# Optimization experiments

Measured on AMD Instinct MI355X. Metric: run time of the kernel, lower is better.

## Reference

```python
import jax, jax.numpy as jnp
import numpy as np

N_NODES = 100000
N_EDGES = 1600000
IN_DIM = 128
OUT_DIM = 64


def setup_inputs() -> dict:
    key = jax.random.key(0)
    k1, k2, k3, k4, k5 = jax.random.split(key, 5)
    return {
        "h_init": jax.random.normal(k1, (N_NODES, IN_DIM), dtype=jnp.float32),
        "W1": jax.random.normal(k2, (OUT_DIM, IN_DIM), dtype=jnp.float32),
        "a": jax.random.normal(k3, (1, OUT_DIM), dtype=jnp.float32),
        "src": jax.random.randint(k4, (N_EDGES,), 0, N_NODES, dtype=jnp.int64)
        if jax.config.jax_enable_x64 else jax.random.randint(k4, (N_EDGES,), 0, N_NODES, dtype=jnp.int32),
        "dst": jax.random.randint(k5, (N_EDGES,), 0, N_NODES, dtype=jnp.int32),
    }


def reference(h_init, W1, a, src, dst):
    N = h_init.shape[0]
    # node projection: [N, out_dim]
    h = h_init @ W1.T
    # per-edge diff feature: dst minus src (DGL edges.dst['h'] - edges.src['h'])
    diff = h[dst] - h[src]                       # [E, out_dim]
    e = jnp.tanh(diff @ a[0])                    # [E] edge attention logit
    # segment softmax over incoming edges of each destination node
    seg_max = jax.ops.segment_max(e, dst, num_segments=N)   # [N]
    ex = jnp.exp(e - seg_max[dst])               # [E]
    denom = jax.ops.segment_sum(ex, dst, num_segments=N)    # [N]
    alpha = ex / denom[dst]                      # [E]
    # weighted sum of diff features per destination node
    h_diff = jax.ops.segment_sum(alpha[:, None] * diff, dst, num_segments=N)  # [N, out_dim]
    return jax.nn.relu(h + h_diff)
```

## Files before the change

kernel.cpp:

```cpp
#include <hip/hip_runtime.h>
#include <hip/hip_fp16.h>

#define N_NODES 100000
#define N_EDGES 1600000
#define IN_DIM 128
#define OUT_DIM 64

#define PROJ_BLKS 1563

#define NB2 782
#define MAXB2 2560
#define CUR_STRIDE 16

#define BIN_NBLK 250
#define BIN_CHUNK 6400
#define BIN_THREADS 1024

#define SG_THREADS 512

typedef short short8 __attribute__((ext_vector_type(8)));
typedef float f32x4 __attribute__((ext_vector_type(4)));

__device__ __forceinline__ short bf16_trunc(float x) {
  return (short)(__float_as_uint(x) >> 16);
}
__device__ __forceinline__ float bf16_tof(short s) {
  return __uint_as_float(((unsigned)(unsigned short)s) << 16);
}
__device__ __forceinline__ float edge_ex(float p) {
  float t2 = __expf(2.f * p);
  float th = 1.f - 2.f * __builtin_amdgcn_rcpf(t2 + 1.f);
  return __expf(th);
}

__global__ __launch_bounds__(256) void fat1_kernel(
    const float* __restrict__ h_init, const float* __restrict__ W1,
    const float* __restrict__ a, float* __restrict__ h,
    __half* __restrict__ h16, float* __restrict__ ha) {
  __shared__ short whi[16 * 64 * 8];
  __shared__ short wlo[16 * 64 * 8];

  for (int idx = threadIdx.x; idx < 16 * 64; idx += 256) {
    int f = idx >> 6;
    int l = idx & 63;
    int kc = f >> 2, ot = f & 3;
    const float* wsrc =
        W1 + (ot * 16 + (l & 15)) * IN_DIM + kc * 32 + (l >> 4) * 8;
    short hi[8], lo[8];
#pragma unroll
    for (int j = 0; j < 8; j++) {
      float x = wsrc[j];
      short hv = bf16_trunc(x);
      hi[j] = hv;
      lo[j] = bf16_trunc(x - bf16_tof(hv));
    }
    *(short8*)&whi[idx * 8] = *(const short8*)hi;
    *(short8*)&wlo[idx * 8] = *(const short8*)lo;
  }

  int row0 = blockIdx.x * 64;
  int w = threadIdx.x >> 6;
  int l = threadIdx.x & 63;
  int m = l & 15;
  int q = l >> 4;

  int arow = row0 + w * 16 + m;
  if (arow >= N_NODES) arow = N_NODES - 1;
  const float* xsrc = h_init + (size_t)arow * IN_DIM + q * 8;

  short8 ahi[4], alo[4];
#pragma unroll
  for (int kc = 0; kc < 4; kc++) {
    float xv[8];
    *(float4*)&xv[0] = *(const float4*)(xsrc + kc * 32);
    *(float4*)&xv[4] = *(const float4*)(xsrc + kc * 32 + 4);
    short hi[8], lo[8];
#pragma unroll
    for (int j = 0; j < 8; j++) {
      short hv = bf16_trunc(xv[j]);
      hi[j] = hv;
      lo[j] = bf16_trunc(xv[j] - bf16_tof(hv));
    }
    ahi[kc] = *(const short8*)hi;
    alo[kc] = *(const short8*)lo;
  }
  __syncthreads();

  f32x4 acc[4] = {{0.f, 0.f, 0.f, 0.f},
                  {0.f, 0.f, 0.f, 0.f},
                  {0.f, 0.f, 0.f, 0.f},
                  {0.f, 0.f, 0.f, 0.f}};

#pragma unroll
  for (int kc = 0; kc < 4; kc++) {
#pragma unroll
    for (int ot = 0; ot < 4; ot++) {
      int base = (((kc << 2) | ot) * 64 + l) * 8;
      short8 bhi = *(const short8*)&whi[base];
      short8 blo = *(const short8*)&wlo[base];
      acc[ot] = __builtin_amdgcn_mfma_f32_16x16x32_bf16(ahi[kc], bhi, acc[ot],
                                                        0, 0, 0);
      acc[ot] = __builtin_amdgcn_mfma_f32_16x16x32_bf16(ahi[kc], blo, acc[ot],
                                                        0, 0, 0);
      acc[ot] = __builtin_amdgcn_mfma_f32_16x16x32_bf16(alo[kc], bhi, acc[ot],
                                                        0, 0, 0);
    }
  }

  float pa[4] = {0.f, 0.f, 0.f, 0.f};
#pragma unroll
  for (int ot = 0; ot < 4; ot++) {
    float aval = a[ot * 16 + m];
#pragma unroll
    for (int r = 0; r < 4; r++) pa[r] += acc[ot][r] * aval;
  }
  int rowb = row0 + w * 16 + q * 4;
#pragma unroll
  for (int r = 0; r < 4; r++) {
    int row = rowb + r;
    if (row < N_NODES) {
#pragma unroll
      for (int ot = 0; ot < 4; ot++) {
        h[(size_t)row * OUT_DIM + ot * 16 + m] = acc[ot][r];
        h16[(size_t)row * OUT_DIM + ot * 16 + m] = __float2half(acc[ot][r]);
      }
    }
  }
#pragma unroll
  for (int r = 0; r < 4; r++) {
    pa[r] += __shfl_xor(pa[r], 1);
    pa[r] += __shfl_xor(pa[r], 2);
    pa[r] += __shfl_xor(pa[r], 4);
    pa[r] += __shfl_xor(pa[r], 8);
  }
  if (m == 0) {
#pragma unroll
    for (int r = 0; r < 4; r++) {
      int row = rowb + r;
      if (row < N_NODES) ha[row] = pa[r];
    }
  }
}

__global__ __launch_bounds__(BIN_THREADS) void bin_scatter_kernel(
    const int* __restrict__ src, const int* __restrict__ dst,
    int* __restrict__ bucket_cursor, unsigned int* __restrict__ pairs) {
  __shared__ int hst[NB2];
  __shared__ int cur[NB2];
  __shared__ int dlds[BIN_CHUNK];
  int t = threadIdx.x;
  for (int i = t; i < NB2; i += BIN_THREADS) hst[i] = 0;
  __syncthreads();
  int beg = blockIdx.x * BIN_CHUNK;
  for (int e = t; e < BIN_CHUNK; e += BIN_THREADS) {
    int d = dst[beg + e];
    dlds[e] = d;
    atomicAdd(&hst[d >> 7], 1);
  }
  __syncthreads();
  for (int i = t; i < NB2; i += BIN_THREADS) {
    int c = hst[i];
    cur[i] =
        (c > 0) ? atomicAdd(&bucket_cursor[i * CUR_STRIDE], c) + i * MAXB2 : 0;
  }
  __syncthreads();
  for (int e = t; e < BIN_CHUNK; e += BIN_THREADS) {
    int d = dlds[e];
    int pos = atomicAdd(&cur[d >> 7], 1);
    pairs[pos] = ((unsigned int)src[beg + e] << 7) | (unsigned int)(d & 127);
  }
}

__global__ __launch_bounds__(SG_THREADS) void sortgather_kernel(
    const float* __restrict__ h, const __half* __restrict__ h16,
    const float* __restrict__ ha, const int* __restrict__ bucket_cursor,
    const unsigned int* __restrict__ pairs, float* __restrict__ out) {
  __shared__ unsigned int plds[MAXB2];
  __shared__ int2 slds[MAXB2];
  __shared__ float had[128];
  __shared__ int hist[128];
  __shared__ int scn[128];
  __shared__ int cur[128];
  int b = blockIdx.x;
  int t = threadIdx.x;
  int node0 = b << 7;
  int cnt = min(bucket_cursor[b * CUR_STRIDE], MAXB2);

  if (t < 128) {
    int node = node0 + t;
    had[t] = (node < N_NODES) ? ha[node] : 0.f;
    hist[t] = 0;
  }
  __syncthreads();
  for (int i = t; i < cnt; i += SG_THREADS) {
    unsigned int p = pairs[(size_t)b * MAXB2 + i];
    plds[i] = p;
    atomicAdd(&hist[p & 127u], 1);
  }
  __syncthreads();
  int v = (t < 128) ? hist[t] : 0;
  if (t < 128) scn[t] = v;
  __syncthreads();
  for (int off = 1; off < 128; off <<= 1) {
    int u = (t >= off && t < 128) ? scn[t - off] : 0;
    __syncthreads();
    if (t < 128) scn[t] += u;
    __syncthreads();
  }
  if (t < 128) cur[t] = scn[t] - v;
  __syncthreads();
  for (int i = t; i < cnt; i += SG_THREADS) {
    unsigned int p = plds[i];
    int nl = (int)(p & 127u);
    int sb = (int)(p & 0xFFFFFF80u);
    float ex = edge_ex(had[nl] - ha[sb >> 7]);
    int pos = atomicAdd(&cur[nl], 1);
    slds[pos] = make_int2(sb, __float_as_int(ex));
  }
  __syncthreads();

  int wv = t >> 6;
  int lane = t & 63;
  int g = lane >> 3;
  int l8 = lane & 7;
  const char* h16b = (const char*)h16;
  const float4* h4 = (const float4*)h;
  float4* o4 = (float4*)out;

  for (int nl = wv; nl < 128; nl += 8) {
    int node = node0 + nl;
    if (node >= N_NODES) break;
    int endp = scn[nl];
    int begp = endp - hist[nl];
    float4 hd0 = h4[(size_t)node * (OUT_DIM / 4) + l8 * 2];
    float4 hd1 = h4[(size_t)node * (OUT_DIM / 4) + l8 * 2 + 1];
    float acc[8] = {0.f, 0.f, 0.f, 0.f, 0.f, 0.f, 0.f, 0.f};
    float den = 0.f;
    int last = endp - 1;

    for (int i0 = begp + g; i0 < endp; i0 += 32) {
      int2 e[4];
      float exv[4];
#pragma unroll
      for (int k = 0; k < 4; k++) {
        int i = i0 + k * 8;
        e[k] = slds[i < endp ? i : last];
        exv[k] = (i < endp) ? __int_as_float(e[k].y) : 0.f;
      }
      uint4 uv[4];
#pragma unroll
      for (int k = 0; k < 4; k++)
        uv[k] = *(const uint4*)(h16b + e[k].x + (l8 << 4));
#pragma unroll
      for (int k = 0; k < 4; k++) {
        union {
          uint4 u;
          __half hh[8];
        } U;
        U.u = uv[k];
        float ex = exv[k];
        den += ex;
#pragma unroll
        for (int j = 0; j < 8; j++)
          acc[j] = fmaf(__half2float(U.hh[j]), ex, acc[j]);
      }
    }

#pragma unroll
    for (int j = 0; j < 8; j++) {
      acc[j] += __shfl_xor(acc[j], 8);
      acc[j] += __shfl_xor(acc[j], 16);
      acc[j] += __shfl_xor(acc[j], 32);
    }
    den += __shfl_xor(den, 8);
    den += __shfl_xor(den, 16);
    den += __shfl_xor(den, 32);

    if (g == 0) {
      bool has = den > 0.f;
      float inv = has ? __builtin_amdgcn_rcpf(den) : 0.f;
      float4 r0, r1;
      r0.x = fmaxf(has ? 2.f * hd0.x - acc[0] * inv : hd0.x, 0.f);
      r0.y = fmaxf(has ? 2.f * hd0.y - acc[1] * inv : hd0.y, 0.f);
      r0.z = fmaxf(has ? 2.f * hd0.z - acc[2] * inv : hd0.z, 0.f);
      r0.w = fmaxf(has ? 2.f * hd0.w - acc[3] * inv : hd0.w, 0.f);
      r1.x = fmaxf(has ? 2.f * hd1.x - acc[4] * inv : hd1.x, 0.f);
      r1.y = fmaxf(has ? 2.f * hd1.y - acc[5] * inv : hd1.y, 0.f);
      r1.z = fmaxf(has ? 2.f * hd1.z - acc[6] * inv : hd1.z, 0.f);
      r1.w = fmaxf(has ? 2.f * hd1.w - acc[7] * inv : hd1.w, 0.f);
      o4[(size_t)node * (OUT_DIM / 4) + l8 * 2] = r0;
      o4[(size_t)node * (OUT_DIM / 4) + l8 * 2 + 1] = r1;
    }
  }
}

extern "C" void kernel_launch(void* const* d_in, const int* in_sizes, int n_in,
                              void* d_out, int out_size, void* d_ws,
                              size_t ws_size, hipStream_t stream) {
  const float* h_init = (const float*)d_in[0];
  const float* W1 = (const float*)d_in[1];
  const float* a = (const float*)d_in[2];
  const int* src = (const int*)d_in[3];
  const int* dst = (const int*)d_in[4];
  float* out = (float*)d_out;

  float* h = (float*)d_ws;
  __half* h16 = (__half*)(h + (size_t)N_NODES * OUT_DIM);
  float* ha = (float*)(h16 + (size_t)N_NODES * OUT_DIM);
  unsigned int* pairs = (unsigned int*)(ha + N_NODES);
  int* bucket_cursor = (int*)(pairs + (size_t)NB2 * MAXB2);

  hipMemsetAsync(bucket_cursor, 0, NB2 * CUR_STRIDE * sizeof(int), stream);
  fat1_kernel<<<PROJ_BLKS, 256, 0, stream>>>(h_init, W1, a, h, h16, ha);
  bin_scatter_kernel<<<BIN_NBLK, BIN_THREADS, 0, stream>>>(src, dst,
                                                           bucket_cursor,
                                                           pairs);
  sortgather_kernel<<<NB2, SG_THREADS, 0, stream>>>(h, h16, ha, bucket_cursor,
                                                    pairs, out);
}
```

Before: 204.7 us.

## Fuse edge binning into projection kernel with per-block fixed-capacity runs

```diff
diff --git a/kernel.cpp b/kernel.cpp
--- a/kernel.cpp
+++ b/kernel.cpp
@@ -10,11 +10,13 @@
 
 #define NB2 782
 #define MAXB2 2560
-#define CUR_STRIDE 16
-
-#define BIN_NBLK 250
-#define BIN_CHUNK 6400
-#define BIN_THREADS 1024
+
+#define BIN_NBLK 100
+#define BIN_CHUNK 16000
+#define RUNCAP 64
+#define RUNTOT (BIN_NBLK * RUNCAP)
+
+#define PB_GRID (PROJ_BLKS + BIN_NBLK)
 
 #define SG_THREADS 512
 
@@ -33,12 +35,43 @@
   return __expf(th);
 }
 
-__global__ __launch_bounds__(256) void fat1_kernel(
+__global__ __launch_bounds__(256) void fused_pb_kernel(
     const float* __restrict__ h_init, const float* __restrict__ W1,
-    const float* __restrict__ a, float* __restrict__ h,
-    __half* __restrict__ h16, float* __restrict__ ha) {
-  __shared__ short whi[16 * 64 * 8];
-  __shared__ short wlo[16 * 64 * 8];
+    const float* __restrict__ a, const int* __restrict__ src,
+    const int* __restrict__ dst, float* __restrict__ h,
+    __half* __restrict__ h16, float* __restrict__ ha,
+    unsigned int* __restrict__ pairs, unsigned char* __restrict__ cnt8) {
+  __shared__ __align__(16) char smem[16 * 64 * 8 * 2 * sizeof(short)];
+
+  if (blockIdx.x < BIN_NBLK) {
+    int* cur = (int*)smem;
+    int qb = blockIdx.x;
+    for (int i = threadIdx.x; i < NB2; i += 256) cur[i] = 0;
+    __syncthreads();
+    int beg = qb * BIN_CHUNK;
+    for (int e0 = threadIdx.x * 4; e0 < BIN_CHUNK; e0 += 256 * 4) {
+      int4 s4 = *(const int4*)&src[beg + e0];
+      int4 d4 = *(const int4*)&dst[beg + e0];
+      int ss[4] = {s4.x, s4.y, s4.z, s4.w};
+      int dd[4] = {d4.x, d4.y, d4.z, d4.w};
+#pragma unroll
+      for (int k = 0; k < 4; k++) {
+        int b = dd[k] >> 7;
+        int idx = atomicAdd(&cur[b], 1);
+        if (idx < RUNCAP)
+          pairs[(size_t)b * RUNTOT + qb * RUNCAP + idx] =
+              ((unsigned)ss[k] << 7) | (unsigned)(dd[k] & 127);
+      }
+    }
+    __syncthreads();
+    for (int i = threadIdx.x; i < NB2; i += 256)
+      cnt8[qb * NB2 + i] = (unsigned char)min(cur[i], RUNCAP);
+    return;
+  }
+
+  int pb = blockIdx.x - BIN_NBLK;
+  short* whi = (short*)smem;
+  short* wlo = whi + 16 * 64 * 8;
 
   for (int idx = threadIdx.x; idx < 16 * 64; idx += 256) {
     int f = idx >> 6;
@@ -58,7 +91,7 @@
     *(short8*)&wlo[idx * 8] = *(const short8*)lo;
   }
 
-  int row0 = blockIdx.x * 64;
+  int row0 = pb * 64;
   int w = threadIdx.x >> 6;
   int l = threadIdx.x & 63;
   int m = l & 15;
@@ -142,38 +175,9 @@
   }
 }
 
-__global__ __launch_bounds__(BIN_THREADS) void bin_scatter_kernel(
-    const int* __restrict__ src, const int* __restrict__ dst,
-    int* __restrict__ bucket_cursor, unsigned int* __restrict__ pairs) {
-  __shared__ int hst[NB2];
-  __shared__ int cur[NB2];
-  __shared__ int dlds[BIN_CHUNK];
-  int t = threadIdx.x;
-  for (int i = t; i < NB2; i += BIN_THREADS) hst[i] = 0;
-  __syncthreads();
-  int beg = blockIdx.x * BIN_CHUNK;
-  for (int e = t; e < BIN_CHUNK; e += BIN_THREADS) {
-    int d = dst[beg + e];
-    dlds[e] = d;
-    atomicAdd(&hst[d >> 7], 1);
-  }
-  __syncthreads();
-  for (int i = t; i < NB2; i += BIN_THREADS) {
-    int c = hst[i];
-    cur[i] =
-        (c > 0) ? atomicAdd(&bucket_cursor[i * CUR_STRIDE], c) + i * MAXB2 : 0;
-  }
-  __syncthreads();
-  for (int e = t; e < BIN_CHUNK; e += BIN_THREADS) {
-    int d = dlds[e];
-    int pos = atomicAdd(&cur[d >> 7], 1);
-    pairs[pos] = ((unsigned int)src[beg + e] << 7) | (unsigned int)(d & 127);
-  }
-}
-
 __global__ __launch_bounds__(SG_THREADS) void sortgather_kernel(
     const float* __restrict__ h, const __half* __restrict__ h16,
-    const float* __restrict__ ha, const int* __restrict__ bucket_cursor,
+    const float* __restrict__ ha, const unsigned char* __restrict__ cnt8,
     const unsigned int* __restrict__ pairs, float* __restrict__ out) {
   __shared__ unsigned int plds[MAXB2];
   __shared__ int2 slds[MAXB2];
@@ -181,23 +185,35 @@
   __shared__ int hist[128];
   __shared__ int scn[128];
   __shared__ int cur[128];
+  __shared__ int cntv[BIN_NBLK];
+  __shared__ int tot;
   int b = blockIdx.x;
   int t = threadIdx.x;
   int node0 = b << 7;
-  int cnt = min(bucket_cursor[b * CUR_STRIDE], MAXB2);
-
+
+  if (t == 0) tot = 0;
+  if (t < BIN_NBLK) cntv[t] = cnt8[t * NB2 + b];
   if (t < 128) {
     int node = node0 + t;
     had[t] = (node < N_NODES) ? ha[node] : 0.f;
     hist[t] = 0;
   }
   __syncthreads();
-  for (int i = t; i < cnt; i += SG_THREADS) {
-    unsigned int p = pairs[(size_t)b * MAXB2 + i];
-    plds[i] = p;
-    atomicAdd(&hist[p & 127u], 1);
-  }
-  __syncthreads();
+
+  for (int i = t; i < RUNTOT; i += SG_THREADS) {
+    int qb = i >> 6;
+    if ((i & (RUNCAP - 1)) < cntv[qb]) {
+      unsigned int p = pairs[(size_t)b * RUNTOT + i];
+      int pos = atomicAdd(&tot, 1);
+      if (pos < MAXB2) {
+        plds[pos] = p;
+        atomicAdd(&hist[p & 127u], 1);
+      }
+    }
+  }
+  __syncthreads();
+  int cnt = min(tot, MAXB2);
+
   int v = (t < 128) ? hist[t] : 0;
   if (t < 128) scn[t] = v;
   __syncthreads();
@@ -308,13 +324,11 @@
   __half* h16 = (__half*)(h + (size_t)N_NODES * OUT_DIM);
   float* ha = (float*)(h16 + (size_t)N_NODES * OUT_DIM);
   unsigned int* pairs = (unsigned int*)(ha + N_NODES);
-  int* bucket_cursor = (int*)(pairs + (size_t)NB2 * MAXB2);
-
-  hipMemsetAsync(bucket_cursor, 0, NB2 * CUR_STRIDE * sizeof(int), stream);
-  fat1_kernel<<<PROJ_BLKS, 256, 0, stream>>>(h_init, W1, a, h, h16, ha);
-  bin_scatter_kernel<<<BIN_NBLK, BIN_THREADS, 0, stream>>>(src, dst,
-                                                           bucket_cursor,
-                                                           pairs);
-  sortgather_kernel<<<NB2, SG_THREADS, 0, stream>>>(h, h16, ha, bucket_cursor,
-                                                    pairs, out);
-}
+  unsigned char* cnt8 =
+      (unsigned char*)(pairs + (size_t)NB2 * RUNTOT);
+
+  fused_pb_kernel<<<PB_GRID, 256, 0, stream>>>(h_init, W1, a, src, dst, h, h16,
+                                               ha, pairs, cnt8);
+  sortgather_kernel<<<NB2, SG_THREADS, 0, stream>>>(h, h16, ha, cnt8, pairs,
+                                                    out);
+}
```

Result: slower. 217.2 us (+6.1%).

## Drop fp32 h buffer and assign one 8-lane group per destination node

Applied to the files above, without the earlier changes.

```diff
diff --git a/kernel.cpp b/kernel.cpp
--- a/kernel.cpp
+++ b/kernel.cpp
@@ -35,8 +35,8 @@
 
 __global__ __launch_bounds__(256) void fat1_kernel(
     const float* __restrict__ h_init, const float* __restrict__ W1,
-    const float* __restrict__ a, float* __restrict__ h,
-    __half* __restrict__ h16, float* __restrict__ ha) {
+    const float* __restrict__ a, __half* __restrict__ h16,
+    float* __restrict__ ha) {
   __shared__ short whi[16 * 64 * 8];
   __shared__ short wlo[16 * 64 * 8];
 
@@ -120,10 +120,8 @@
     int row = rowb + r;
     if (row < N_NODES) {
 #pragma unroll
-      for (int ot = 0; ot < 4; ot++) {
-        h[(size_t)row * OUT_DIM + ot * 16 + m] = acc[ot][r];
+      for (int ot = 0; ot < 4; ot++)
         h16[(size_t)row * OUT_DIM + ot * 16 + m] = __float2half(acc[ot][r]);
-      }
     }
   }
 #pragma unroll
@@ -172,9 +170,9 @@
 }
 
 __global__ __launch_bounds__(SG_THREADS) void sortgather_kernel(
-    const float* __restrict__ h, const __half* __restrict__ h16,
-    const float* __restrict__ ha, const int* __restrict__ bucket_cursor,
-    const unsigned int* __restrict__ pairs, float* __restrict__ out) {
+    const __half* __restrict__ h16, const float* __restrict__ ha,
+    const int* __restrict__ bucket_cursor, const unsigned int* __restrict__
+        pairs, float* __restrict__ out) {
   __shared__ unsigned int plds[MAXB2];
   __shared__ int2 slds[MAXB2];
   __shared__ float had[128];
@@ -219,31 +217,31 @@
   }
   __syncthreads();
 
-  int wv = t >> 6;
-  int lane = t & 63;
-  int g = lane >> 3;
-  int l8 = lane & 7;
+  int sg = t >> 3;
+  int l8 = t & 7;
   const char* h16b = (const char*)h16;
-  const float4* h4 = (const float4*)h;
   float4* o4 = (float4*)out;
 
-  for (int nl = wv; nl < 128; nl += 8) {
+  for (int nl = sg; nl < 128; nl += 64) {
     int node = node0 + nl;
-    if (node >= N_NODES) break;
+    if (node >= N_NODES) continue;
     int endp = scn[nl];
     int begp = endp - hist[nl];
-    float4 hd0 = h4[(size_t)node * (OUT_DIM / 4) + l8 * 2];
-    float4 hd1 = h4[(size_t)node * (OUT_DIM / 4) + l8 * 2 + 1];
+    union {
+      uint4 u;
+      __half hh[8];
+    } HD;
+    HD.u = *(const uint4*)(h16b + ((size_t)node << 7) + (l8 << 4));
     float acc[8] = {0.f, 0.f, 0.f, 0.f, 0.f, 0.f, 0.f, 0.f};
     float den = 0.f;
     int last = endp - 1;
 
-    for (int i0 = begp + g; i0 < endp; i0 += 32) {
+    for (int base = begp; base < endp; base += 4) {
       int2 e[4];
       float exv[4];
 #pragma unroll
       for (int k = 0; k < 4; k++) {
-        int i = i0 + k * 8;
+        int i = base + k;
         e[k] = slds[i < endp ? i : last];
         exv[k] = (i < endp) ? __int_as_float(e[k].y) : 0.f;
       }
@@ -266,31 +264,22 @@
       }
     }
 
-#pragma unroll
-    for (int j = 0; j < 8; j++) {
-      acc[j] += __shfl_xor(acc[j], 8);
-      acc[j] += __shfl_xor(acc[j], 16);
-      acc[j] += __shfl_xor(acc[j], 32);
-    }
-    den += __shfl_xor(den, 8);
-    den += __shfl_xor(den, 16);
-    den += __shfl_xor(den, 32);
-
-    if (g == 0) {
-      bool has = den > 0.f;
-      float inv = has ? __builtin_amdgcn_rcpf(den) : 0.f;
-      float4 r0, r1;
-      r0.x = fmaxf(has ? 2.f * hd0.x - acc[0] * inv : hd0.x, 0.f);
-      r0.y = fmaxf(has ? 2.f * hd0.y - acc[1] * inv : hd0.y, 0.f);
-      r0.z = fmaxf(has ? 2.f * hd0.z - acc[2] * inv : hd0.z, 0.f);
-      r0.w = fmaxf(has ? 2.f * hd0.w - acc[3] * inv : hd0.w, 0.f);
-      r1.x = fmaxf(has ? 2.f * hd1.x - acc[4] * inv : hd1.x, 0.f);
-      r1.y = fmaxf(has ? 2.f * hd1.y - acc[5] * inv : hd1.y, 0.f);
-      r1.z = fmaxf(has ? 2.f * hd1.z - acc[6] * inv : hd1.z, 0.f);
-      r1.w = fmaxf(has ? 2.f * hd1.w - acc[7] * inv : hd1.w, 0.f);
-      o4[(size_t)node * (OUT_DIM / 4) + l8 * 2] = r0;
-      o4[(size_t)node * (OUT_DIM / 4) + l8 * 2 + 1] = r1;
-    }
+    bool has = den > 0.f;
+    float inv = has ? __builtin_amdgcn_rcpf(den) : 0.f;
+    float hd[8];
+#pragma unroll
+    for (int j = 0; j < 8; j++) hd[j] = __half2float(HD.hh[j]);
+    float4 r0, r1;
+    r0.x = fmaxf(has ? 2.f * hd[0] - acc[0] * inv : hd[0], 0.f);
+    r0.y = fmaxf(has ? 2.f * hd[1] - acc[1] * inv : hd[1], 0.f);
+    r0.z = fmaxf(has ? 2.f * hd[2] - acc[2] * inv : hd[2], 0.f);
+    r0.w = fmaxf(has ? 2.f * hd[3] - acc[3] * inv : hd[3], 0.f);
+    r1.x = fmaxf(has ? 2.f * hd[4] - acc[4] * inv : hd[4], 0.f);
+    r1.y = fmaxf(has ? 2.f * hd[5] - acc[5] * inv : hd[5], 0.f);
+    r1.z = fmaxf(has ? 2.f * hd[6] - acc[6] * inv : hd[6], 0.f);
+    r1.w = fmaxf(has ? 2.f * hd[7] - acc[7] * inv : hd[7], 0.f);
+    o4[(size_t)node * (OUT_DIM / 4) + l8 * 2] = r0;
+    o4[(size_t)node * (OUT_DIM / 4) + l8 * 2 + 1] = r1;
   }
 }
 
@@ -304,17 +293,16 @@
   const int* dst = (const int*)d_in[4];
   float* out = (float*)d_out;
 
-  float* h = (float*)d_ws;
-  __half* h16 = (__half*)(h + (size_t)N_NODES * OUT_DIM);
+  __half* h16 = (__half*)d_ws;
   float* ha = (float*)(h16 + (size_t)N_NODES * OUT_DIM);
   unsigned int* pairs = (unsigned int*)(ha + N_NODES);
   int* bucket_cursor = (int*)(pairs + (size_t)NB2 * MAXB2);
 
   hipMemsetAsync(bucket_cursor, 0, NB2 * CUR_STRIDE * sizeof(int), stream);
-  fat1_kernel<<<PROJ_BLKS, 256, 0, stream>>>(h_init, W1, a, h, h16, ha);
+  fat1_kernel<<<PROJ_BLKS, 256, 0, stream>>>(h_init, W1, a, h16, ha);
   bin_scatter_kernel<<<BIN_NBLK, BIN_THREADS, 0, stream>>>(src, dst,
                                                            bucket_cursor,
                                                            pairs);
-  sortgather_kernel<<<NB2, SG_THREADS, 0, stream>>>(h, h16, ha, bucket_cursor,
+  sortgather_kernel<<<NB2, SG_THREADS, 0, stream>>>(h16, ha, bucket_cursor,
                                                     pairs, out);
 }
```

New measurement: 183.0 us. -10.6%, faster.
